# Performance work log

Hardware: AMD Instinct MI355X
Metric: run time of the kernel (lower is better)

## Reference

```python
import jax, jax.numpy as jnp
import numpy as np

N = 50000
E = 800000
C = 64


def setup_inputs() -> dict:
    key = jax.random.key(0)
    ks = jax.random.split(key, 16)
    s = 0.05
    x = jax.random.normal(ks[0], (N, C), jnp.float32)
    edge_attr = jax.random.uniform(ks[1], (E, 4), dtype=jnp.float32)
    edge_index = jax.random.randint(ks[2], (2, E), 0, N)
    deg_hist = jax.random.uniform(ks[3], (N,), dtype=jnp.float32) * 32.0
    W = jax.random.normal(ks[4], (C, C), jnp.float32) * s          # self.weight[0]
    We = jax.random.normal(ks[5], (3, C), jnp.float32) * s         # edge_encoder
    be = jnp.zeros((C,), jnp.float32)
    Wpre = jax.random.normal(ks[6], (3 * C, C), jnp.float32) * s   # pre_nn Linear
    bpre = jnp.zeros((C,), jnp.float32)
    A_S = 4 * 3  # aggregators * scalers
    Wpost = jax.random.normal(ks[7], ((A_S + 1) * C, C), jnp.float32) * s
    bpost = jnp.zeros((C,), jnp.float32)
    Wih = jax.random.normal(ks[8], (C, 3 * C), jnp.float32) * s    # GRUCell input weights (transposed)
    bih = jnp.zeros((3 * C,), jnp.float32)
    Whh = jax.random.normal(ks[9], (C, 3 * C), jnp.float32) * s    # GRUCell hidden weights (transposed)
    bhh = jnp.zeros((3 * C,), jnp.float32)
    return dict(x=x, edge_attr=edge_attr, deg_hist=deg_hist, W=W, We=We, be=be,
                Wpre=Wpre, bpre=bpre, Wpost=Wpost, bpost=bpost,
                Wih=Wih, bih=bih, Whh=Whh, bhh=bhh, edge_index=edge_index)


def reference(x, edge_attr, deg_hist, W, We, be, Wpre, bpre, Wpost, bpost,
              Wih, bih, Whh, bhh, edge_index):
    n_nodes = x.shape[0]
    # gated path: m = x @ weight[0]
    m = x @ W  # [N, C]
    src, dst = edge_index[0], edge_index[1]
    # message: edge-weight scaling + edge encoder + pre-MLP (single Linear)
    ew = edge_attr[:, 3:4]                         # [E, 1]
    ea = edge_attr[:, :3] @ We + be                # [E, C]
    xi = ew * m[dst]                               # x_i (target)
    xj = ew * m[src]                               # x_j (source)
    ea = ew * ea
    h = jnp.concatenate([xi, xj, ea], axis=-1) @ Wpre + bpre  # [E, C]
    # multi-aggregator scatter: mean, min, max, std (keyed by target node)
    ones = jnp.ones((h.shape[0],), h.dtype)
    cnt = jax.ops.segment_sum(ones, dst, num_segments=n_nodes)       # [N]
    safe = jnp.maximum(cnt, 1.0)[:, None]
    s1 = jax.ops.segment_sum(h, dst, num_segments=n_nodes)
    s2 = jax.ops.segment_sum(h * h, dst, num_segments=n_nodes)
    mean = s1 / safe
    mean_sq = s2 / safe
    std = jnp.sqrt(jax.nn.relu(mean_sq - mean * mean) + 1e-5)
    has = (cnt > 0)[:, None]
    mn = jnp.where(has, jax.ops.segment_min(h, dst, num_segments=n_nodes), 0.0)
    mx = jnp.where(has, jax.ops.segment_max(h, dst, num_segments=n_nodes), 0.0)
    agg = jnp.concatenate([mean, mn, mx, std], axis=-1)  # [N, 4C]
    # degree scalers (faithfully replicating the cumulative reassignment in the torch loop)
    deg = jnp.maximum(cnt, 1.0)[:, None]
    avg_log = jnp.mean(jnp.log(deg_hist + 1.0))
    logd = jnp.log(deg + 1.0)
    o1 = agg                          # identity
    o2 = o1 * (logd / avg_log)        # amplification
    o3 = o2 * (avg_log / logd)        # attenuation applied on top of o2 (torch bug, kept)
    out = jnp.concatenate([o1, o2, o3], axis=-1)          # [N, 12C]
    # post-MLP on cat([m, aggregated])
    out = jnp.concatenate([m, out], axis=-1) @ Wpost + bpost  # [N, C]
    # GRUCell(out, x): torch gate order r, z, n
    gi = out @ Wih + bih
    gh = x @ Whh + bhh
    ir, iz, i_n = jnp.split(gi, 3, axis=-1)
    hr, hz, h_n = jnp.split(gh, 3, axis=-1)
    r = jax.nn.sigmoid(ir + hr)
    z = jax.nn.sigmoid(iz + hz)
    n = jnp.tanh(i_n + r * h_n)
    return (1.0 - z) * n + z * x
```

## Files before the change

kernel.cpp:

```cpp
#include <hip/hip_runtime.h>
#include <math.h>

#define NN  50000
#define NNP 50048
#define NE  800000

#define B_BG1   0u
#define B_BG2A  49152u
#define B_BG2B  90112u
#define B_BG3   122880u
#define B_WE2   147456u
#define B_BE2   148224u
#define B_B3    148480u
#define B_SUML  149248u
#define B_XB    149504u
#define B_NF    6555648u
#define B_GH    19367936u
#define B_A2    38586368u
#define B_S2F   70617088u
#define B_CNT   70817280u
#define B_OFFS  71017280u
#define B_CUR   71217408u
#define B_EL2   71417856u
#define B_PART  77817856u

#define SCAN_B  196

typedef __attribute__((ext_vector_type(8))) short s8v;
typedef __attribute__((ext_vector_type(4))) float f4v;

__device__ inline short f2b(float f){
    union { float f; unsigned u; } v; v.f = f;
    unsigned r = v.u + 0x7fffu + ((v.u >> 16) & 1u);
    return (short)(r >> 16);
}
__device__ inline float b2f(short b){
    union { unsigned u; float f; } v; v.u = ((unsigned)(unsigned short)b) << 16;
    return v.f;
}

__global__ __launch_bounds__(256) void k_prep(const float* __restrict__ x,
    const float* __restrict__ dh, const int* __restrict__ dstA,
    const float* __restrict__ W, const float* __restrict__ Wpre,
    const float* __restrict__ We, const float* __restrict__ be,
    const float* __restrict__ bpost, const float* __restrict__ Wpost,
    const float* __restrict__ Wih, const float* __restrict__ bih,
    const float* __restrict__ Whh, int* __restrict__ cnt,
    unsigned char* __restrict__ wsb)
{
    __shared__ float sred[4];
    int b = blockIdx.x, t = threadIdx.x;
    atomicAdd(&cnt[dstA[b * 256 + t]], 1);

    if (b < 38) {
        int idx = b * 256 + t;
        if (idx < 3072) {
            short* dst = (short*)(wsb + B_BG1);
            int lane = idx & 63, ts = idx >> 6;
            int tt = ts >> 1, s = ts & 1;
            int quad = lane >> 4, l15 = lane & 15, n = tt*16 + l15;
            for (int j = 0; j < 8; ++j) {
                int k = s*32 + quad*8 + j;
                float v;
                if (n < 64)       v = W[k*64 + n];
                else if (n < 128) { v = 0.f; for (int c = 0; c < 64; ++c) v += W[k*64+c]*Wpre[c*64 + (n-64)]; }
                else if (n < 192) { v = 0.f; for (int c = 0; c < 64; ++c) v += W[k*64+c]*Wpre[4096 + c*64 + (n-128)]; }
                else              v = Whh[k*192 + (n-192)];
                dst[((size_t)ts*64 + lane)*8 + j] = f2b(v);
            }
        } else if (idx < 5632) {
            int id = idx - 3072;
            short* dst = (short*)(wsb + B_BG2A);
            int lane = id & 63, ts = id >> 6;
            int quad = lane >> 4, l15 = lane & 15;
            int tt = ts / 10, s = ts % 10;
            int n = tt*16 + l15;
            for (int j = 0; j < 8; ++j) {
                int k = s*32 + quad*8 + j;
                float v = Wpost[k*64 + n];
                if (k >= 64) v += Wpost[(k + 512)*64 + n];
                dst[((size_t)ts*64 + lane)*8 + j] = f2b(v);
            }
        } else if (idx < 7680) {
            int id = idx - 5632;
            short* dst = (short*)(wsb + B_BG2B);
            int lane = id & 63, ts = id >> 6;
            int quad = lane >> 4, l15 = lane & 15;
            int tt = ts / 8, s = ts % 8;
            int n = tt*16 + l15;
            for (int j = 0; j < 8; ++j) {
                int k = s*32 + quad*8 + j;
                dst[((size_t)ts*64 + lane)*8 + j] = f2b(Wpost[(320 + k)*64 + n]);
            }
        } else if (idx < 9216) {
            int id = idx - 7680;
            short* dst = (short*)(wsb + B_BG3);
            int lane = id & 63, ts = id >> 6;
            int tt = ts >> 1, s = ts & 1;
            int quad = lane >> 4, l15 = lane & 15, n = tt*16 + l15;
            for (int j = 0; j < 8; ++j) {
                int k = s*32 + quad*8 + j;
                dst[((size_t)ts*64 + lane)*8 + j] = f2b(Wih[k*192 + n]);
            }
        } else if (idx < 9408) {
            int t2 = idx - 9216; int kk = t2 >> 6, j = t2 & 63;
            float v = 0.f;
            for (int c = 0; c < 64; ++c) v += We[kk*64 + c] * Wpre[(128+c)*64 + j];
            ((float*)(wsb + B_WE2))[t2] = v;
        } else if (idx < 9472) {
            int j = idx - 9408;
            float v = 0.f;
            for (int c = 0; c < 64; ++c) v += be[c] * Wpre[(128+c)*64 + j];
            ((float*)(wsb + B_BE2))[j] = v;
        } else if (idx < 9664) {
            int j = idx - 9472;
            float v = bih[j];
            for (int k = 0; k < 64; ++k) v += bpost[k] * Wih[k*192 + j];
            ((float*)(wsb + B_B3))[j] = v;
        }
    } else if (b < 1601) {
        int i = (b - 38) * 256 + t;
        if (i < 400000) {
            const float4* xp = (const float4*)(x + (size_t)i * 8);
            float4 p0 = xp[0], p1 = xp[1];
            s8v o;
            o[0]=f2b(p0.x); o[1]=f2b(p0.y); o[2]=f2b(p0.z); o[3]=f2b(p0.w);
            o[4]=f2b(p1.x); o[5]=f2b(p1.y); o[6]=f2b(p1.z); o[7]=f2b(p1.w);
            *(s8v*)((short*)(wsb + B_XB) + (size_t)i * 8) = o;
        }
    } else if (b < 1797) {
        int i = (b - 1601) * 256 + t;
        float v = (i < NN) ? logf(dh[i] + 1.f) : 0.f;
        #pragma unroll
        for (int m = 32; m >= 1; m >>= 1) v += __shfl_xor(v, m, 64);
        if ((t & 63) == 0) sred[t >> 6] = v;
        __syncthreads();
        if (t == 0) atomicAdd((float*)(wsb + B_SUML), sred[0]+sred[1]+sred[2]+sred[3]);
    }
}

__global__ __launch_bounds__(256) void k_scanA(const int* __restrict__ cnt,
    int* __restrict__ loc, int* __restrict__ part)
{
    __shared__ int sh[256];
    int t = threadIdx.x, i = blockIdx.x * 256 + t;
    int v = (i < NN) ? cnt[i] : 0;
    sh[t] = v; __syncthreads();
    #pragma unroll
    for (int o = 1; o < 256; o <<= 1) {
        int u = (t >= o) ? sh[t - o] : 0;
        __syncthreads();
        sh[t] += u;
        __syncthreads();
    }
    if (i < NN) loc[i] = sh[t] - v;
    if (t == 255) part[blockIdx.x] = sh[255];
}

__global__ __launch_bounds__(256) void k_scanB(int* __restrict__ part,
    int* __restrict__ offs)
{
    __shared__ int sh[256];
    int t = threadIdx.x;
    int v = (t < SCAN_B) ? part[t] : 0;
    sh[t] = v; __syncthreads();
    #pragma unroll
    for (int o = 1; o < 256; o <<= 1) {
        int u = (t >= o) ? sh[t - o] : 0;
        __syncthreads();
        sh[t] += u;
        __syncthreads();
    }
    if (t < SCAN_B) part[t] = sh[t] - v;
    if (t == 255) offs[NN] = sh[255];
}

__global__ __launch_bounds__(256) void k_scanC(const int* __restrict__ part,
    int* __restrict__ loc, int* __restrict__ offs, int* __restrict__ cur)
{
    int i = blockIdx.x * 256 + threadIdx.x;
    if (i < NN) {
        int v = loc[i] + part[blockIdx.x];
        offs[i] = v; cur[i] = v;
    }
}

__global__ void k_scatter(const int* __restrict__ srcA, const int* __restrict__ dstA,
                          int* __restrict__ cur, int2* __restrict__ el2)
{
    int e = blockIdx.x * 256 + threadIdx.x;
    if (e < NE) {
        int p = atomicAdd(&cur[dstA[e]], 1);
        el2[p] = make_int2(e, srcA[e]);
    }
}

__global__ __launch_bounds__(256) void k_g1(unsigned char* __restrict__ wsb)
{
    const short* xb = (const short*)(wsb + B_XB);
    const short* bf = (const short*)(wsb + B_BG1);
    short* a2 = (short*)(wsb + B_A2);
    short* nf = (short*)(wsb + B_NF);
    short* gh = (short*)(wsb + B_GH);
    int w = threadIdx.x >> 6, lane = threadIdx.x & 63;
    int quad = lane >> 4, l15 = lane & 15;
    int R0 = blockIdx.x * 64 + w * 16;
    const short* arow = xb + (size_t)(R0 + l15) * 64 + quad * 8;
    s8v a0 = *(const s8v*)(arow);
    s8v a1 = *(const s8v*)(arow + 32);
    f4v acc[24];
    #pragma unroll
    for (int t = 0; t < 24; ++t) acc[t] = (f4v){0.f,0.f,0.f,0.f};
    #pragma unroll
    for (int t = 0; t < 24; ++t) {
        s8v b0 = *(const s8v*)(bf + ((size_t)(t*2+0)*64 + lane)*8);
        s8v b1 = *(const s8v*)(bf + ((size_t)(t*2+1)*64 + lane)*8);
        acc[t] = __builtin_amdgcn_mfma_f32_16x16x32_bf16(a0, b0, acc[t], 0, 0, 0);
        acc[t] = __builtin_amdgcn_mfma_f32_16x16x32_bf16(a1, b1, acc[t], 0, 0, 0);
    }
    #pragma unroll
    for (int t = 0; t < 24; ++t) {
        #pragma unroll
        for (int r = 0; r < 4; ++r) {
            int row = R0 + quad*4 + r;
            if (row >= NN) continue;
            short v = f2b(acc[t][r]);
            if (t < 4)       a2[(size_t)row*320 + t*16 + l15] = v;
            else if (t < 12) nf[(size_t)row*128 + (t-4)*16 + l15] = v;
            else             gh[(size_t)row*192 + (t-12)*16 + l15] = v;
        }
    }
}

__global__ __launch_bounds__(256) void k_agg(const float* __restrict__ eattr,
    const float* __restrict__ bpre, unsigned char* __restrict__ wsb)
{
    __shared__ float4 sEA[4][64];
    __shared__ int    sOFF[4][64];
    int lane = threadIdx.x & 63;
    int w    = threadIdx.x >> 6;
    int wid  = blockIdx.x * 4 + w;
    const int* offs = (const int*)(wsb + B_OFFS);
    const int2* el2 = (const int2*)(wsb + B_EL2);
    const unsigned char* nfb = wsb + B_NF;
    const short* nf = (const short*)(wsb + B_NF);
    const float* we2p = (const float*)(wsb + B_WE2);
    float we0 = we2p[lane], we1 = we2p[64 + lane], we2v = we2p[128 + lane];
    float be2l = ((const float*)(wsb + B_BE2))[lane];
    float bprel = bpre[lane];
    float rcpavg = (float)NN / ((const float*)(wsb + B_SUML))[0];
    const float4* e4 = (const float4*)eattr;
    unsigned laneoff = 128u + 2u * (unsigned)lane;
    short* a2b = (short*)(wsb + B_A2);
    float* s2f = (float*)(wsb + B_S2F);

    for (int n = wid; n < NN; n += 8192) {
        float md2l = b2f(nf[(size_t)n * 128 + lane]);
        float tbase = md2l + be2l;
        int o0 = offs[n], o1e = offs[n + 1];
        float s = 0.f, ss = 0.f, mn = INFINITY, mx = -INFINITY;
        for (int base = o0; base < o1e; base += 64) {
            int cnt = o1e - base; if (cnt > 64) cnt = 64;
            if (lane < cnt) {
                int2 es = el2[base + lane];
                sOFF[w][lane] = es.y << 8;
                sEA[w][lane]  = e4[es.x];
            }
            for (int d0 = 0; d0 < cnt; d0 += 8) {
                float msv[8];
                #pragma unroll
                for (int u = 0; u < 8; ++u) {
                    int d = d0 + u; if (d > cnt - 1) d = cnt - 1;
                    unsigned off = (unsigned)sOFF[w][d] + laneoff;
                    msv[u] = b2f(*(const short*)(nfb + off));
                }
                #pragma unroll
                for (int u = 0; u < 8; ++u) {
                    int d = d0 + u;
                    if (d < cnt) {
                        float4 ea = sEA[w][d];
                        float t = tbase + msv[u];
                        t = fmaf(ea.x, we0, t);
                        t = fmaf(ea.y, we1, t);
                        t = fmaf(ea.z, we2v, t);
                        float h = fmaf(ea.w, t, bprel);
                        s += h; ss = fmaf(h, h, ss);
                        mn = fminf(mn, h); mx = fmaxf(mx, h);
                    }
                }
            }
        }
        int deg = o1e - o0;
        float safe = (float)(deg > 0 ? deg : 1);
        float mean = s / safe;
        float var  = ss / safe - mean * mean;
        float stdv = sqrtf(fmaxf(var, 0.f) + 1e-5f);
        if (deg == 0) { mn = 0.f; mx = 0.f; }
        short* a2r = a2b + (size_t)n * 320;
        a2r[ 64 + lane] = f2b(mean); a2r[128 + lane] = f2b(mn);
        a2r[192 + lane] = f2b(mx);   a2r[256 + lane] = f2b(stdv);
        if (lane == 0) s2f[n] = logf(safe + 1.f) * rcpavg;
    }
}

__global__ __launch_bounds__(256) void k_g23(const float* __restrict__ x,
    const float* __restrict__ bhh, unsigned char* __restrict__ wsb,
    float* __restrict__ out)
{
    __shared__ short sm[64 * 72];
    __shared__ float sS2[64];
    const short* a2  = (const short*)(wsb + B_A2);
    const short* bgA = (const short*)(wsb + B_BG2A);
    const short* bgB = (const short*)(wsb + B_BG2B);
    const short* bg3 = (const short*)(wsb + B_BG3);
    const short* gh  = (const short*)(wsb + B_GH);
    const float* b3  = (const float*)(wsb + B_B3);
    const float* s2f = (const float*)(wsb + B_S2F);
    int w = threadIdx.x >> 6, lane = threadIdx.x & 63;
    int quad = lane >> 4, l15 = lane & 15;
    int R0 = blockIdx.x * 64 + w * 16;

    {
        int i = threadIdx.x;
        if (i < 64) {
            int row = blockIdx.x * 64 + i;
            sS2[i] = (row < NN) ? s2f[row] : 0.f;
        }
    }

    const short* aBase = a2 + (size_t)(R0 + l15) * 320 + quad * 8;
    f4v acc1[4], acc2[4];
    #pragma unroll
    for (int t = 0; t < 4; ++t) { acc1[t] = (f4v){0.f,0.f,0.f,0.f}; acc2[t] = (f4v){0.f,0.f,0.f,0.f}; }
    #pragma unroll 2
    for (int s = 0; s < 10; ++s) {
        s8v a = *(const s8v*)(aBase + s * 32);
        #pragma unroll
        for (int t = 0; t < 4; ++t) {
            s8v b = *(const s8v*)(bgA + ((size_t)(t*10 + s)*64 + lane)*8);
            acc1[t] = __builtin_amdgcn_mfma_f32_16x16x32_bf16(a, b, acc1[t], 0, 0, 0);
        }
    }
    #pragma unroll 2
    for (int s = 0; s < 8; ++s) {
        s8v a = *(const s8v*)(aBase + 64 + s * 32);
        #pragma unroll
        for (int t = 0; t < 4; ++t) {
            s8v b = *(const s8v*)(bgB + ((size_t)(t*8 + s)*64 + lane)*8);
            acc2[t] = __builtin_amdgcn_mfma_f32_16x16x32_bf16(a, b, acc2[t], 0, 0, 0);
        }
    }
    __syncthreads();
    #pragma unroll
    for (int t = 0; t < 4; ++t)
        #pragma unroll
        for (int r = 0; r < 4; ++r) {
            int lr = w*16 + quad*4 + r;
            float v = acc1[t][r] + sS2[lr] * acc2[t][r];
            sm[lr * 72 + t*16 + l15] = f2b(v);
        }
    __syncthreads();

    const short* arow = sm + (w*16 + l15) * 72 + quad * 8;
    s8v a0 = *(const s8v*)(arow);
    s8v a1 = *(const s8v*)(arow + 32);
    f4v acc[12];
    #pragma unroll
    for (int t = 0; t < 12; ++t) acc[t] = (f4v){0.f,0.f,0.f,0.f};
    #pragma unroll
    for (int t = 0; t < 12; ++t) {
        s8v b0 = *(const s8v*)(bg3 + ((size_t)(t*2+0)*64 + lane)*8);
        s8v b1 = *(const s8v*)(bg3 + ((size_t)(t*2+1)*64 + lane)*8);
        acc[t] = __builtin_amdgcn_mfma_f32_16x16x32_bf16(a0, b0, acc[t], 0, 0, 0);
        acc[t] = __builtin_amdgcn_mfma_f32_16x16x32_bf16(a1, b1, acc[t], 0, 0, 0);
    }
    #pragma unroll
    for (int t = 0; t < 4; ++t) {
        #pragma unroll
        for (int r = 0; r < 4; ++r) {
            int row = R0 + quad*4 + r;
            if (row >= NN) continue;
            int c = t*16 + l15;
            float ir  = acc[t][r]   + b3[c];
            float iz  = acc[t+4][r] + b3[64 + c];
            float inn = acc[t+8][r] + b3[128 + c];
            const short* g = gh + (size_t)row * 192;
            float hr = b2f(g[c])       + bhh[c];
            float hz = b2f(g[64 + c])  + bhh[64 + c];
            float hn = b2f(g[128 + c]) + bhh[128 + c];
            float rr = 1.f / (1.f + expf(-(ir + hr)));
            float zz = 1.f / (1.f + expf(-(iz + hz)));
            float nn = tanhf(inn + rr * hn);
            out[(size_t)row*64 + c] = (1.f - zz)*nn + zz*x[(size_t)row*64 + c];
        }
    }
}

extern "C" void kernel_launch(void* const* d_in, const int* in_sizes, int n_in,
                              void* d_out, int out_size, void* d_ws, size_t ws_size,
                              hipStream_t stream)
{
    const float* x     = (const float*)d_in[0];
    const float* eattr = (const float*)d_in[1];
    const float* dh    = (const float*)d_in[2];
    const float* W     = (const float*)d_in[3];
    const float* We    = (const float*)d_in[4];
    const float* be    = (const float*)d_in[5];
    const float* Wpre  = (const float*)d_in[6];
    const float* bpre  = (const float*)d_in[7];
    const float* Wpost = (const float*)d_in[8];
    const float* bpost = (const float*)d_in[9];
    const float* Wih   = (const float*)d_in[10];
    const float* bih   = (const float*)d_in[11];
    const float* Whh   = (const float*)d_in[12];
    const float* bhh   = (const float*)d_in[13];
    const int*   eidx  = (const int*)d_in[14];
    unsigned char* wsb = (unsigned char*)d_ws;
    float* out = (float*)d_out;
    const int* srcA = eidx;
    const int* dstA = eidx + NE;
    int* cnt  = (int*)(wsb + B_CNT);
    int* offs = (int*)(wsb + B_OFFS);
    int* cur  = (int*)(wsb + B_CUR);
    int2* el2 = (int2*)(wsb + B_EL2);
    int* part = (int*)(wsb + B_PART);

    hipMemsetAsync(wsb + B_SUML, 0, 4, stream);
    hipMemsetAsync(cnt, 0, NN * sizeof(int), stream);

    k_prep    <<<3125, 256, 0, stream>>>(x, dh, dstA, W, Wpre, We, be, bpost,
                                         Wpost, Wih, bih, Whh, cnt, wsb);
    k_scanA   <<<SCAN_B, 256, 0, stream>>>(cnt, cur, part);
    k_scanB   <<<1, 256, 0, stream>>>(part, offs);
    k_scanC   <<<SCAN_B, 256, 0, stream>>>(part, cur, offs, cur);
    k_scatter <<<NE/256, 256, 0, stream>>>(srcA, dstA, cur, el2);
    k_g1      <<<NNP/64, 256, 0, stream>>>(wsb);
    k_agg     <<<2048, 256, 0, stream>>>(eattr, bpre, wsb);
    k_g23     <<<NNP/64, 256, 0, stream>>>(x, bhh, wsb, out);
}
```

Baseline: 296.6 us.

## Record edge ranks during counting, merge scan passes, and vectorize aggregate stores

Result: faster. 256.5 us (-13.5%).

```diff
diff --git a/kernel.cpp b/kernel.cpp
--- a/kernel.cpp
+++ b/kernel.cpp
@@ -20,13 +20,14 @@
 #define B_S2F   70617088u
 #define B_CNT   70817280u
 #define B_OFFS  71017280u
-#define B_CUR   71217408u
-#define B_EL2   71417856u
-#define B_PART  77817856u
+#define B_RANK  71217408u
+#define B_EL2   74417408u
+#define B_PART  80817408u
 
 #define SCAN_B  196
 
 typedef __attribute__((ext_vector_type(8))) short s8v;
+typedef __attribute__((ext_vector_type(4))) short s4v;
 typedef __attribute__((ext_vector_type(4))) float f4v;
 
 __device__ inline short f2b(float f){
@@ -46,11 +47,14 @@
     const float* __restrict__ bpost, const float* __restrict__ Wpost,
     const float* __restrict__ Wih, const float* __restrict__ bih,
     const float* __restrict__ Whh, int* __restrict__ cnt,
-    unsigned char* __restrict__ wsb)
+    int* __restrict__ rank, unsigned char* __restrict__ wsb)
 {
     __shared__ float sred[4];
     int b = blockIdx.x, t = threadIdx.x;
-    atomicAdd(&cnt[dstA[b * 256 + t]], 1);
+    {
+        int e = b * 256 + t;
+        rank[e] = atomicAdd(&cnt[dstA[e]], 1);
+    }
 
     if (b < 38) {
         int idx = b * 256 + t;
@@ -77,8 +81,13 @@
             int n = tt*16 + l15;
             for (int j = 0; j < 8; ++j) {
                 int k = s*32 + quad*8 + j;
-                float v = Wpost[k*64 + n];
-                if (k >= 64) v += Wpost[(k + 512)*64 + n];
+                float v;
+                if (k < 64) v = Wpost[k*64 + n];
+                else {
+                    int kk = k - 64, ch = kk >> 2, st = kk & 3;
+                    int ok = 64 + st*64 + ch;
+                    v = Wpost[ok*64 + n] + Wpost[(ok + 512)*64 + n];
+                }
                 dst[((size_t)ts*64 + lane)*8 + j] = f2b(v);
             }
         } else if (idx < 7680) {
@@ -90,7 +99,9 @@
             int n = tt*16 + l15;
             for (int j = 0; j < 8; ++j) {
                 int k = s*32 + quad*8 + j;
-                dst[((size_t)ts*64 + lane)*8 + j] = f2b(Wpost[(320 + k)*64 + n]);
+                int ch = k >> 2, st = k & 3;
+                int ok = 320 + st*64 + ch;
+                dst[((size_t)ts*64 + lane)*8 + j] = f2b(Wpost[ok*64 + n]);
             }
         } else if (idx < 9216) {
             int id = idx - 7680;
@@ -140,7 +151,7 @@
 }
 
 __global__ __launch_bounds__(256) void k_scanA(const int* __restrict__ cnt,
-    int* __restrict__ loc, int* __restrict__ part)
+    int* __restrict__ offs, int* __restrict__ part)
 {
     __shared__ int sh[256];
     int t = threadIdx.x, i = blockIdx.x * 256 + t;
@@ -153,15 +164,15 @@
         sh[t] += u;
         __syncthreads();
     }
-    if (i < NN) loc[i] = sh[t] - v;
+    if (i < NN) offs[i] = sh[t] - v;
     if (t == 255) part[blockIdx.x] = sh[255];
 }
 
-__global__ __launch_bounds__(256) void k_scanB(int* __restrict__ part,
+__global__ __launch_bounds__(256) void k_scanC(const int* __restrict__ part,
     int* __restrict__ offs)
 {
     __shared__ int sh[256];
-    int t = threadIdx.x;
+    int b = blockIdx.x, t = threadIdx.x;
     int v = (t < SCAN_B) ? part[t] : 0;
     sh[t] = v; __syncthreads();
     #pragma unroll
@@ -171,28 +182,21 @@
         sh[t] += u;
         __syncthreads();
     }
-    if (t < SCAN_B) part[t] = sh[t] - v;
-    if (t == 255) offs[NN] = sh[255];
-}
-
-__global__ __launch_bounds__(256) void k_scanC(const int* __restrict__ part,
-    int* __restrict__ loc, int* __restrict__ offs, int* __restrict__ cur)
-{
-    int i = blockIdx.x * 256 + threadIdx.x;
-    if (i < NN) {
-        int v = loc[i] + part[blockIdx.x];
-        offs[i] = v; cur[i] = v;
-    }
-}
-
-__global__ void k_scatter(const int* __restrict__ srcA, const int* __restrict__ dstA,
-                          int* __restrict__ cur, int2* __restrict__ el2)
+    int base = (b == 0) ? 0 : sh[b - 1];
+    int i = b * 256 + t;
+    if (i < NN) offs[i] += base;
+    if (b == 0 && t == 0) offs[NN] = NE;
+}
+
+__global__ __launch_bounds__(256) void k_scatter(const int* __restrict__ srcA,
+    const int* __restrict__ dstA, const int* __restrict__ rank,
+    const int* __restrict__ offs, int2* __restrict__ el2)
 {
     int e = blockIdx.x * 256 + threadIdx.x;
-    if (e < NE) {
-        int p = atomicAdd(&cur[dstA[e]], 1);
-        el2[p] = make_int2(e, srcA[e]);
-    }
+    int dst = dstA[e];
+    int r   = rank[e];
+    int src = srcA[e];
+    el2[offs[dst] + r] = make_int2(e, src);
 }
 
 __global__ __launch_bounds__(256) void k_g1(unsigned char* __restrict__ wsb)
@@ -296,9 +300,8 @@
         float var  = ss / safe - mean * mean;
         float stdv = sqrtf(fmaxf(var, 0.f) + 1e-5f);
         if (deg == 0) { mn = 0.f; mx = 0.f; }
-        short* a2r = a2b + (size_t)n * 320;
-        a2r[ 64 + lane] = f2b(mean); a2r[128 + lane] = f2b(mn);
-        a2r[192 + lane] = f2b(mx);   a2r[256 + lane] = f2b(stdv);
+        s4v o; o[0] = f2b(mean); o[1] = f2b(mn); o[2] = f2b(mx); o[3] = f2b(stdv);
+        *(s4v*)(a2b + (size_t)n * 320 + 64 + (lane << 2)) = o;
         if (lane == 0) s2f[n] = logf(safe + 1.f) * rcpavg;
     }
 }
@@ -421,7 +424,7 @@
     const int* dstA = eidx + NE;
     int* cnt  = (int*)(wsb + B_CNT);
     int* offs = (int*)(wsb + B_OFFS);
-    int* cur  = (int*)(wsb + B_CUR);
+    int* rank = (int*)(wsb + B_RANK);
     int2* el2 = (int2*)(wsb + B_EL2);
     int* part = (int*)(wsb + B_PART);
 
@@ -429,11 +432,10 @@
     hipMemsetAsync(cnt, 0, NN * sizeof(int), stream);
 
     k_prep    <<<3125, 256, 0, stream>>>(x, dh, dstA, W, Wpre, We, be, bpost,
-                                         Wpost, Wih, bih, Whh, cnt, wsb);
-    k_scanA   <<<SCAN_B, 256, 0, stream>>>(cnt, cur, part);
-    k_scanB   <<<1, 256, 0, stream>>>(part, offs);
-    k_scanC   <<<SCAN_B, 256, 0, stream>>>(part, cur, offs, cur);
-    k_scatter <<<NE/256, 256, 0, stream>>>(srcA, dstA, cur, el2);
+                                         Wpost, Wih, bih, Whh, cnt, rank, wsb);
+    k_scanA   <<<SCAN_B, 256, 0, stream>>>(cnt, offs, part);
+    k_scanC   <<<SCAN_B, 256, 0, stream>>>(part, offs);
+    k_scatter <<<NE/256, 256, 0, stream>>>(srcA, dstA, rank, offs, el2);
     k_g1      <<<NNP/64, 256, 0, stream>>>(wsb);
     k_agg     <<<2048, 256, 0, stream>>>(eattr, bpre, wsb);
     k_g23     <<<NNP/64, 256, 0, stream>>>(x, bhh, wsb, out);
```
